# Optimization experiments

Hardware: AMD Instinct MI355X
Metric: run time of the kernel (lower is better)

## Reference

```python
import jax, jax.numpy as jnp
import numpy as np

F_NODES = 360        # nodes per graph == num_features (square connectome)
NUM_GRAPHS = 128
NUM_EDGES = 1_000_000
C = 128              # hidden_channels
NUM_LAYERS = 3
HIDDEN = 512
NUM_CLASSES = 2
EPS = 1e-5


def _bn(x, g, b):
    # BatchNorm1d in training mode: biased batch statistics over the batch dim.
    m = x.mean(axis=0)
    v = x.var(axis=0)
    return (x - m) * jax.lax.rsqrt(v + EPS) * g + b


def _gcn(x, W, b, src, dst):
    # GCNConv: x' = D^{-1/2} (A + I) D^{-1/2} (x W) + b
    N = x.shape[0]
    h = x @ W                                   # [N, C]
    loop = jnp.arange(N, dtype=src.dtype)
    src2 = jnp.concatenate([src, loop])
    dst2 = jnp.concatenate([dst, loop])
    deg = jax.ops.segment_sum(jnp.ones_like(dst2, dtype=h.dtype), dst2, num_segments=N)
    dinv = jnp.where(deg > 0, jax.lax.rsqrt(deg), 0.0)
    norm = dinv[src2] * dinv[dst2]              # [E+N]
    out = jax.ops.segment_sum(h[src2] * norm[:, None], dst2, num_segments=N)
    return out + b


def setup_inputs() -> dict:
    key = jax.random.key(0)
    ks = jax.random.split(key, 16)
    N = NUM_GRAPHS * F_NODES
    x = jax.random.normal(ks[0], (N, F_NODES), jnp.float32)
    # edges confined within each graph
    g = jax.random.randint(ks[1], (NUM_EDGES,), 0, NUM_GRAPHS)
    edge_src = g * F_NODES + jax.random.randint(ks[2], (NUM_EDGES,), 0, F_NODES)
    edge_dst = g * F_NODES + jax.random.randint(ks[3], (NUM_EDGES,), 0, F_NODES)
    batch = jnp.repeat(jnp.arange(NUM_GRAPHS), F_NODES)

    def lin(k, fi, fo):
        s = 1.0 / np.sqrt(fi)
        return jax.random.uniform(k, (fi, fo), jnp.float32, -s, s)

    input_dim = F_NODES * (F_NODES + 1) // 2    # 64980
    input_dim1 = input_dim + C * NUM_LAYERS     # 65364
    H2 = HIDDEN // 2
    params = dict(
        Wc1=lin(ks[4], F_NODES, C), bc1=jnp.zeros((C,), jnp.float32),
        Wc2=lin(ks[5], C, C), bc2=jnp.zeros((C,), jnp.float32),
        Wc3=lin(ks[6], C, C), bc3=jnp.zeros((C,), jnp.float32),
        bn_g=jnp.ones((input_dim,), jnp.float32), bn_b=jnp.zeros((input_dim,), jnp.float32),
        bnh_g=jnp.ones((C * NUM_LAYERS,), jnp.float32), bnh_b=jnp.zeros((C * NUM_LAYERS,), jnp.float32),
        W1=lin(ks[7], input_dim1, HIDDEN), b1=jnp.zeros((HIDDEN,), jnp.float32),
        g1=jnp.ones((HIDDEN,), jnp.float32), be1=jnp.zeros((HIDDEN,), jnp.float32),
        W2=lin(ks[8], HIDDEN, H2), b2=jnp.zeros((H2,), jnp.float32),
        g2=jnp.ones((H2,), jnp.float32), be2=jnp.zeros((H2,), jnp.float32),
        W3=lin(ks[9], H2, H2), b3=jnp.zeros((H2,), jnp.float32),
        g3=jnp.ones((H2,), jnp.float32), be3=jnp.zeros((H2,), jnp.float32),
        W4=lin(ks[10], H2, NUM_CLASSES), b4=jnp.zeros((NUM_CLASSES,), jnp.float32),
    )
    return {"x": x, "edge_src": edge_src, "edge_dst": edge_dst, "batch": batch, **params}


def reference(x, edge_src, edge_dst, batch,
              Wc1, bc1, Wc2, bc2, Wc3, bc3,
              bn_g, bn_b, bnh_g, bnh_b,
              W1, b1, g1, be1, W2, b2, g2, be2, W3, b3, g3, be3, W4, b4):
    N, F = x.shape
    B = N // F                                   # nodes per graph == F
    # stacked GCN convs with tanh
    xs = [x]
    for W, b in ((Wc1, bc1), (Wc2, bc2), (Wc3, bc3)):
        xs.append(jnp.tanh(_gcn(xs[-1], W, b, edge_src, edge_dst)))
    # per-graph upper-triangular gather of the raw connectome (vectorized)
    iu0, iu1 = np.triu_indices(F)
    x0 = xs[0].reshape(B, F, F)[:, iu0, iu1]     # [B, F(F+1)/2]
    x0 = _bn(x0, bn_g, bn_b)
    # per-layer segment-mean pooling over graphs
    cnt = jax.ops.segment_sum(jnp.ones((N,), x.dtype), batch, num_segments=B)
    h = jnp.concatenate(
        [jax.ops.segment_sum(xx, batch, num_segments=B) / cnt[:, None] for xx in xs[1:]],
        axis=1)                                  # [B, C*num_layers]
    h = _bn(h, bnh_g, bnh_b)
    z = jnp.concatenate([x0, h], axis=1)         # [B, input_dim1]
    # MLP head (dropout in eval mode => identity)
    z = jax.nn.relu(_bn(z @ W1 + b1, g1, be1))
    z = jax.nn.relu(_bn(z @ W2 + b2, g2, be2))
    z = jax.nn.relu(_bn(z @ W3 + b3, g3, be3))
    return jax.nn.log_softmax(z @ W4 + b4, axis=1)
```

## Files before the change

kernel.cpp:

```cpp
#include <hip/hip_runtime.h>
#include <hip/hip_bf16.h>
#include <math.h>

#define FN 360
#define NG 128
#define NN 46080
#define CH 128
#define NE 1000000
#define TRI 64980
#define D1 65364
#define ZLD 65376
#define H1 512
#define H2 256
#define EPS 1e-5f
#define NSPLIT 128

typedef unsigned short u16;
typedef __attribute__((ext_vector_type(8))) short bf16x8;
typedef __attribute__((ext_vector_type(4))) float f32x4;

__device__ __forceinline__ float bf2f(u16 v) {
  union { unsigned u; float f; } x; x.u = ((unsigned)v) << 16; return x.f;
}
__device__ __forceinline__ u16 f2bf(float f) {
  union { float f; unsigned u; } x; x.f = f;
  unsigned r = x.u + 0x7fffu + ((x.u >> 16) & 1u);
  return (u16)(r >> 16);
}
__device__ __forceinline__ bf16x8 bzero8() {
  bf16x8 z;
#pragma unroll
  for (int j = 0; j < 8; j++) z[j] = 0;
  return z;
}

static const size_t A32_OFF  = 0;
static const size_t DINV_OFF = 66355200;
static const size_t Z_OFF    = 66539520;
static const size_t PT_OFF   = 83275776;
static const size_t H1_OFF   = 95072256;
static const size_t H2_OFF   = 106868736;
static const size_t H3_OFF   = 118665216;
static const size_t HP_OFF   = 130461696;
static const size_t A1_OFF   = 130658304;
static const size_t A2_OFF   = 130789376;
static const size_t A3_OFF   = 130854912;
static const size_t Y1_OFF   = 130920448;
static const size_t PART_OFF = 0;

__global__ void k_deg(const int* __restrict__ dst, float* __restrict__ deg) {
  int e = blockIdx.x * 256 + threadIdx.x;
  if (e < NE) atomicAdd(&deg[dst[e]], 1.0f);
}

__global__ void k_dinv(float* __restrict__ deg) {
  int i = blockIdx.x * 256 + threadIdx.x;
  if (i < NN) deg[i] = rsqrtf(deg[i] + 1.0f);
}

__global__ void k_abuild(const int* __restrict__ src, const int* __restrict__ dst,
                         const float* __restrict__ dinv, float* __restrict__ A) {
  int e = blockIdx.x * 256 + threadIdx.x;
  if (e < NE) {
    int s = src[e], d = dst[e];
    int g = d / FN;
    int ls = s - g * FN, ld = d - g * FN;
    atomicAdd(&A[(size_t)g * FN * FN + (size_t)ld * FN + ls], dinv[s] * dinv[d]);
  } else if (e < NE + NN) {
    int i = e - NE;
    int g = i / FN, l = i - g * FN;
    float dv = dinv[i];
    atomicAdd(&A[(size_t)g * FN * FN + (size_t)l * FN + l], dv * dv);
  }
}

__global__ __launch_bounds__(256) void k_gemm_xw_f32(
    const float* __restrict__ X, const float* __restrict__ W,
    u16* __restrict__ PT, int K) {
  __shared__ __attribute__((aligned(16))) u16 WT[128][40];
  int wid = threadIdx.x >> 6, lane = threadIdx.x & 63;
  int quad = lane >> 4, l16 = lane & 15;
  int m0 = blockIdx.x * 64 + (wid & 1) * 32;
  int n0w = (wid >> 1) * 64;
  int kl = threadIdx.x >> 3, nseg = (threadIdx.x & 7) * 16;
  f32x4 acc[2][4];
#pragma unroll
  for (int i = 0; i < 2; i++)
#pragma unroll
    for (int j = 0; j < 4; j++) acc[i][j] = (f32x4){0,0,0,0};
  for (int k0 = 0; k0 < K; k0 += 32) {
    __syncthreads();
    int kg = k0 + kl;
    if (kg < K) {
      const float* wrow = W + (size_t)kg * CH + nseg;
      f32x4 w0 = *(const f32x4*)(wrow);
      f32x4 w1 = *(const f32x4*)(wrow + 4);
      f32x4 w2 = *(const f32x4*)(wrow + 8);
      f32x4 w3 = *(const f32x4*)(wrow + 12);
#pragma unroll
      for (int j = 0; j < 4; j++) {
        WT[nseg + j][kl]      = f2bf(w0[j]);
        WT[nseg + 4 + j][kl]  = f2bf(w1[j]);
        WT[nseg + 8 + j][kl]  = f2bf(w2[j]);
        WT[nseg + 12 + j][kl] = f2bf(w3[j]);
      }
    } else {
#pragma unroll
      for (int j = 0; j < 16; j++) WT[nseg + j][kl] = 0;
    }
    __syncthreads();
    int kk = k0 + quad * 8;
    bool kin = kk < K;
    bf16x8 af[2];
#pragma unroll
    for (int tm = 0; tm < 2; tm++) {
      int row = m0 + tm * 16 + l16;
      bf16x8 a = bzero8();
      if (kin) {
        f32x4 va = *(const f32x4*)(X + (size_t)row * K + kk);
        f32x4 vb = *(const f32x4*)(X + (size_t)row * K + kk + 4);
#pragma unroll
        for (int j = 0; j < 4; j++) { a[j] = (short)f2bf(va[j]); a[4 + j] = (short)f2bf(vb[j]); }
      }
      af[tm] = a;
    }
    bf16x8 bfr[4];
#pragma unroll
    for (int tn = 0; tn < 4; tn++)
      bfr[tn] = *(const bf16x8*)&WT[n0w + tn * 16 + l16][quad * 8];
#pragma unroll
    for (int tm = 0; tm < 2; tm++)
#pragma unroll
      for (int tn = 0; tn < 4; tn++)
        acc[tm][tn] = __builtin_amdgcn_mfma_f32_16x16x32_bf16(af[tm], bfr[tn], acc[tm][tn], 0, 0, 0);
  }
#pragma unroll
  for (int tm = 0; tm < 2; tm++)
#pragma unroll
    for (int tn = 0; tn < 4; tn++) {
      int col = n0w + tn * 16 + l16;
      int rowb = m0 + tm * 16 + quad * 4;
#pragma unroll
      for (int r = 0; r < 4; r++) {
        int row = rowb + r;
        int g = row / FN, lr = row - g * FN;
        PT[((size_t)g * CH + col) * FN + lr] = f2bf(acc[tm][tn][r]);
      }
    }
}

__global__ __launch_bounds__(256) void k_gemm_xw_bf16(
    const u16* __restrict__ X, const float* __restrict__ W,
    u16* __restrict__ PT) {
  __shared__ __attribute__((aligned(16))) u16 WT[128][40];
  int wid = threadIdx.x >> 6, lane = threadIdx.x & 63;
  int quad = lane >> 4, l16 = lane & 15;
  int m0 = blockIdx.x * 64 + (wid & 1) * 32;
  int n0w = (wid >> 1) * 64;
  int kl = threadIdx.x >> 3, nseg = (threadIdx.x & 7) * 16;
  f32x4 acc[2][4];
#pragma unroll
  for (int i = 0; i < 2; i++)
#pragma unroll
    for (int j = 0; j < 4; j++) acc[i][j] = (f32x4){0,0,0,0};
  for (int k0 = 0; k0 < CH; k0 += 32) {
    __syncthreads();
    int kg = k0 + kl;
    const float* wrow = W + (size_t)kg * CH + nseg;
    f32x4 w0 = *(const f32x4*)(wrow);
    f32x4 w1 = *(const f32x4*)(wrow + 4);
    f32x4 w2 = *(const f32x4*)(wrow + 8);
    f32x4 w3 = *(const f32x4*)(wrow + 12);
#pragma unroll
    for (int j = 0; j < 4; j++) {
      WT[nseg + j][kl]      = f2bf(w0[j]);
      WT[nseg + 4 + j][kl]  = f2bf(w1[j]);
      WT[nseg + 8 + j][kl]  = f2bf(w2[j]);
      WT[nseg + 12 + j][kl] = f2bf(w3[j]);
    }
    __syncthreads();
    int kk = k0 + quad * 8;
    bf16x8 af[2];
#pragma unroll
    for (int tm = 0; tm < 2; tm++) {
      int row = m0 + tm * 16 + l16;
      af[tm] = *(const bf16x8*)(X + (size_t)row * CH + kk);
    }
    bf16x8 bfr[4];
#pragma unroll
    for (int tn = 0; tn < 4; tn++)
      bfr[tn] = *(const bf16x8*)&WT[n0w + tn * 16 + l16][quad * 8];
#pragma unroll
    for (int tm = 0; tm < 2; tm++)
#pragma unroll
      for (int tn = 0; tn < 4; tn++)
        acc[tm][tn] = __builtin_amdgcn_mfma_f32_16x16x32_bf16(af[tm], bfr[tn], acc[tm][tn], 0, 0, 0);
  }
#pragma unroll
  for (int tm = 0; tm < 2; tm++)
#pragma unroll
    for (int tn = 0; tn < 4; tn++) {
      int col = n0w + tn * 16 + l16;
      int rowb = m0 + tm * 16 + quad * 4;
#pragma unroll
      for (int r = 0; r < 4; r++) {
        int row = rowb + r;
        int g = row / FN, lr = row - g * FN;
        PT[((size_t)g * CH + col) * FN + lr] = f2bf(acc[tm][tn][r]);
      }
    }
}

__global__ __launch_bounds__(256) void k_gemm_agg(
    const float* __restrict__ A32, const u16* __restrict__ PT,
    const float* __restrict__ bias, u16* __restrict__ Hout) {
  int id = blockIdx.x;
  int g = (id & 7) + 8 * (id / 48);
  int mb = (id % 48) >> 3;
  int wid = threadIdx.x >> 6, lane = threadIdx.x & 63;
  int quad = lane >> 4, l16 = lane & 15;
  int m0 = mb * 64 + (wid & 1) * 32;
  int n0 = (wid >> 1) * 64;
  const float* Ag = A32 + (size_t)g * FN * FN;
  const u16* PTg = PT + (size_t)g * CH * FN;
  f32x4 acc[2][4];
#pragma unroll
  for (int i = 0; i < 2; i++)
#pragma unroll
    for (int j = 0; j < 4; j++) acc[i][j] = (f32x4){0,0,0,0};
  for (int k0 = 0; k0 < FN; k0 += 32) {
    int kk = k0 + quad * 8;
    bool kin = kk < FN;
    bf16x8 af[2];
#pragma unroll
    for (int tm = 0; tm < 2; tm++) {
      int row = m0 + tm * 16 + l16;
      bf16x8 a = bzero8();
      if (kin && row < FN) {
        f32x4 va = *(const f32x4*)(Ag + (size_t)row * FN + kk);
        f32x4 vb = *(const f32x4*)(Ag + (size_t)row * FN + kk + 4);
#pragma unroll
        for (int j = 0; j < 4; j++) { a[j] = (short)f2bf(va[j]); a[4 + j] = (short)f2bf(vb[j]); }
      }
      af[tm] = a;
    }
    bf16x8 bfr[4];
#pragma unroll
    for (int tn = 0; tn < 4; tn++) {
      int col = n0 + tn * 16 + l16;
      bfr[tn] = kin ? *(const bf16x8*)(PTg + (size_t)col * FN + kk) : bzero8();
    }
#pragma unroll
    for (int tm = 0; tm < 2; tm++)
#pragma unroll
      for (int tn = 0; tn < 4; tn++)
        acc[tm][tn] = __builtin_amdgcn_mfma_f32_16x16x32_bf16(af[tm], bfr[tn], acc[tm][tn], 0, 0, 0);
  }
#pragma unroll
  for (int tm = 0; tm < 2; tm++)
#pragma unroll
    for (int tn = 0; tn < 4; tn++) {
      int col = n0 + tn * 16 + l16;
      float bc = bias[col];
      int rowb = m0 + tm * 16 + quad * 4;
#pragma unroll
      for (int r = 0; r < 4; r++) {
        int row = rowb + r;
        if (row < FN)
          Hout[(size_t)(g * FN + row) * CH + col] = f2bf(tanhf(acc[tm][tn][r] + bc));
      }
    }
}

__global__ __launch_bounds__(256) void k_gemm_big(
    const u16* __restrict__ Z, const float* __restrict__ W1f, float* __restrict__ part) {
  __shared__ __attribute__((aligned(16))) u16 WT[128][40];
  int id = blockIdx.x;
  int s = (id & 7) + 8 * (id >> 5);
  int n0b = ((id >> 3) & 3) * 128;
  int wid = threadIdx.x >> 6, lane = threadIdx.x & 63;
  int quad = lane >> 4, l16 = lane & 15;
  int m0 = wid * 32;
  int kl = threadIdx.x >> 3, nseg = (threadIdx.x & 7) * 16;
  int kbeg = s * 512;
  int kend = (ZLD < kbeg + 512) ? ZLD : (kbeg + 512);
  f32x4 acc[2][8];
#pragma unroll
  for (int i = 0; i < 2; i++)
#pragma unroll
    for (int j = 0; j < 8; j++) acc[i][j] = (f32x4){0,0,0,0};
  for (int k0 = kbeg; k0 < kend; k0 += 32) {
    __syncthreads();
    int kg = k0 + kl;
    if (kg < D1) {
      const float* wrow = W1f + (size_t)kg * H1 + n0b + nseg;
      f32x4 w0 = *(const f32x4*)(wrow);
      f32x4 w1 = *(const f32x4*)(wrow + 4);
      f32x4 w2 = *(const f32x4*)(wrow + 8);
      f32x4 w3 = *(const f32x4*)(wrow + 12);
#pragma unroll
      for (int j = 0; j < 4; j++) {
        WT[nseg + j][kl]      = f2bf(w0[j]);
        WT[nseg + 4 + j][kl]  = f2bf(w1[j]);
        WT[nseg + 8 + j][kl]  = f2bf(w2[j]);
        WT[nseg + 12 + j][kl] = f2bf(w3[j]);
      }
    } else {
#pragma unroll
      for (int j = 0; j < 16; j++) WT[nseg + j][kl] = 0;
    }
    __syncthreads();
    int kk = k0 + quad * 8;
    bf16x8 af[2];
#pragma unroll
    for (int tm = 0; tm < 2; tm++) {
      int row = m0 + tm * 16 + l16;
      af[tm] = *(const bf16x8*)(Z + (size_t)row * ZLD + kk);
    }
    bf16x8 bfr[8];
#pragma unroll
    for (int tn = 0; tn < 8; tn++)
      bfr[tn] = *(const bf16x8*)&WT[tn * 16 + l16][quad * 8];
#pragma unroll
    for (int tm = 0; tm < 2; tm++)
#pragma unroll
      for (int tn = 0; tn < 8; tn++)
        acc[tm][tn] = __builtin_amdgcn_mfma_f32_16x16x32_bf16(af[tm], bfr[tn], acc[tm][tn], 0, 0, 0);
  }
#pragma unroll
  for (int tm = 0; tm < 2; tm++)
#pragma unroll
    for (int tn = 0; tn < 8; tn++) {
      int col = n0b + tn * 16 + l16;
      int rowb = m0 + tm * 16 + quad * 4;
#pragma unroll
      for (int r = 0; r < 4; r++)
        part[((size_t)s * NG + rowb + r) * H1 + col] = acc[tm][tn][r];
    }
}

__global__ void k_red(const float* __restrict__ part, float* __restrict__ y1) {
  int idx = blockIdx.x * 256 + threadIdx.x;
  float s = 0.f;
#pragma unroll 8
  for (int i = 0; i < NSPLIT; i++) s += part[(size_t)i * 65536 + idx];
  y1[idx] = s;
}

__global__ __launch_bounds__(256) void k_bnrelu(
    const float* __restrict__ y, const float* __restrict__ gam,
    const float* __restrict__ bet, u16* __restrict__ a, int N) {
  __shared__ float sb[4][64], sb2[4][64];
  int c63 = threadIdx.x & 63;
  int grp = threadIdx.x >> 6;
  int c = blockIdx.x * 64 + c63;
  float s = 0.f, ss = 0.f;
#pragma unroll 8
  for (int m = grp * 32; m < grp * 32 + 32; m++) {
    float v = y[(size_t)m * N + c]; s += v; ss += v * v;
  }
  sb[grp][c63] = s; sb2[grp][c63] = ss;
  __syncthreads();
  float S = sb[0][c63] + sb[1][c63] + sb[2][c63] + sb[3][c63];
  float SS = sb2[0][c63] + sb2[1][c63] + sb2[2][c63] + sb2[3][c63];
  float mean = S * (1.0f / NG);
  float var = fmaxf(SS * (1.0f / NG) - mean * mean, 0.f);
  float rstd = rsqrtf(var + EPS);
  float ga = gam[c] * rstd;
  float bb = bet[c] - mean * ga;
#pragma unroll 8
  for (int m = grp * 32; m < grp * 32 + 32; m++) {
    float v = y[(size_t)m * N + c] * ga + bb;
    a[(size_t)m * N + c] = f2bf(fmaxf(v, 0.f));
  }
}

__global__ __launch_bounds__(256) void k_mlpbn(
    const u16* __restrict__ A, const float* __restrict__ W,
    const float* __restrict__ gam, const float* __restrict__ bet,
    u16* __restrict__ aout, int K, int N) {
  __shared__ __attribute__((aligned(16))) u16 WT[64][40];
  __shared__ float rs[4][4][4][16], rss[4][4][4][16];
  int wid = threadIdx.x >> 6, lane = threadIdx.x & 63;
  int quad = lane >> 4, l16 = lane & 15;
  int n0b = blockIdx.x * 64;
  int m0 = wid * 32;
  int kl = threadIdx.x >> 3;
  int nseg = (threadIdx.x & 7) * 8;
  f32x4 acc[2][4];
#pragma unroll
  for (int i = 0; i < 2; i++)
#pragma unroll
    for (int j = 0; j < 4; j++) acc[i][j] = (f32x4){0,0,0,0};
  for (int k0 = 0; k0 < K; k0 += 32) {
    __syncthreads();
    const float* wrow = W + (size_t)(k0 + kl) * N + n0b + nseg;
    f32x4 w0 = *(const f32x4*)(wrow);
    f32x4 w1 = *(const f32x4*)(wrow + 4);
#pragma unroll
    for (int j = 0; j < 4; j++) {
      WT[nseg + j][kl]     = f2bf(w0[j]);
      WT[nseg + 4 + j][kl] = f2bf(w1[j]);
    }
    __syncthreads();
    int kk = k0 + quad * 8;
    bf16x8 af[2];
#pragma unroll
    for (int tm = 0; tm < 2; tm++) {
      int row = m0 + tm * 16 + l16;
      af[tm] = *(const bf16x8*)(A + (size_t)row * K + kk);
    }
    bf16x8 bfr[4];
#pragma unroll
    for (int tn = 0; tn < 4; tn++)
      bfr[tn] = *(const bf16x8*)&WT[tn * 16 + l16][quad * 8];
#pragma unroll
    for (int tm = 0; tm < 2; tm++)
#pragma unroll
      for (int tn = 0; tn < 4; tn++)
        acc[tm][tn] = __builtin_amdgcn_mfma_f32_16x16x32_bf16(af[tm], bfr[tn], acc[tm][tn], 0, 0, 0);
  }
  __syncthreads();
#pragma unroll
  for (int tn = 0; tn < 4; tn++) {
    float s = 0.f, ss = 0.f;
#pragma unroll
    for (int tm = 0; tm < 2; tm++)
#pragma unroll
      for (int r = 0; r < 4; r++) { float v = acc[tm][tn][r]; s += v; ss += v * v; }
    rs[wid][quad][tn][l16] = s;
    rss[wid][quad][tn][l16] = ss;
  }
  __syncthreads();
#pragma unroll
  for (int tn = 0; tn < 4; tn++) {
    float S = 0.f, SS = 0.f;
#pragma unroll
    for (int w = 0; w < 4; w++)
#pragma unroll
      for (int q = 0; q < 4; q++) { S += rs[w][q][tn][l16]; SS += rss[w][q][tn][l16]; }
    float mean = S * (1.0f / NG);
    float var = fmaxf(SS * (1.0f / NG) - mean * mean, 0.f);
    float rstd = rsqrtf(var + EPS);
    int col = n0b + tn * 16 + l16;
    float ga = gam[col] * rstd;
    float bb = bet[col] - mean * ga;
#pragma unroll
    for (int tm = 0; tm < 2; tm++) {
      int rowb = m0 + tm * 16 + quad * 4;
#pragma unroll
      for (int r = 0; r < 4; r++) {
        float v = acc[tm][tn][r] * ga + bb;
        aout[(size_t)(rowb + r) * N + col] = f2bf(fmaxf(v, 0.f));
      }
    }
  }
}

__global__ void k_pool3(const u16* __restrict__ h1, const u16* __restrict__ h2,
                        const u16* __restrict__ h3, float* __restrict__ hp) {
  int g = blockIdx.x, layer = blockIdx.y, c = threadIdx.x;
  const u16* h = (layer == 0) ? h1 : (layer == 1) ? h2 : h3;
  float s = 0.f;
#pragma unroll 8
  for (int r = 0; r < FN; r++) s += bf2f(h[(size_t)(g * FN + r) * CH + c]);
  hp[g * 384 + layer * CH + c] = s * (1.0f / FN);
}

__global__ __launch_bounds__(256) void k_x0bn(
    const float* __restrict__ x, const float* __restrict__ gam,
    const float* __restrict__ bet, const float* __restrict__ hp,
    const float* __restrict__ hgam, const float* __restrict__ hbet,
    u16* __restrict__ z) {
  int i = blockIdx.x;
  if (i < FN) {
    int off = i * FN - (i * (i - 1)) / 2;
    for (int j = i + (int)threadIdx.x; j < FN; j += 256) {
      float s = 0.f, ss = 0.f;
#pragma unroll 8
      for (int b = 0; b < NG; b++) {
        float v = x[(size_t)(b * FN + i) * FN + j];
        s += v; ss += v * v;
      }
      float mean = s * (1.0f / NG);
      float var = fmaxf(ss * (1.0f / NG) - mean * mean, 0.f);
      float rstd = rsqrtf(var + EPS);
      int f = off + (j - i);
      float ga = gam[f] * rstd;
      float bb = bet[f] - mean * ga;
#pragma unroll 8
      for (int b = 0; b < NG; b++) {
        float v = x[(size_t)(b * FN + i) * FN + j];
        z[(size_t)b * ZLD + f] = f2bf(v * ga + bb);
      }
    }
  } else {
    for (int c = threadIdx.x; c < 384; c += 256) {
      float s = 0.f, ss = 0.f;
#pragma unroll 8
      for (int m = 0; m < NG; m++) { float v = hp[m * 384 + c]; s += v; ss += v * v; }
      float mean = s * (1.0f / NG);
      float var = fmaxf(ss * (1.0f / NG) - mean * mean, 0.f);
      float rstd = rsqrtf(var + EPS);
      float ga = hgam[c] * rstd;
      float bb = hbet[c] - mean * ga;
#pragma unroll 8
      for (int m = 0; m < NG; m++)
        z[(size_t)m * ZLD + TRI + c] = f2bf(hp[m * 384 + c] * ga + bb);
    }
    if (threadIdx.x < NG) {
      for (int t = 0; t < ZLD - D1; t++)
        z[(size_t)threadIdx.x * ZLD + D1 + t] = 0;
    }
  }
}

__global__ void k_head(const u16* __restrict__ a3, const float* __restrict__ W4,
                       const float* __restrict__ b4, float* __restrict__ out) {
  __shared__ float w4s[H2 * 2];
  int m = threadIdx.x;
  for (int i = m; i < H2 * 2; i += 128) w4s[i] = W4[i];
  __syncthreads();
  float a0 = b4[0], a1 = b4[1];
  for (int k0 = 0; k0 < H2; k0 += 8) {
    bf16x8 v = *(const bf16x8*)(a3 + (size_t)m * H2 + k0);
#pragma unroll
    for (int j = 0; j < 8; j++) {
      float f = bf2f((u16)v[j]);
      a0 += f * w4s[(k0 + j) * 2];
      a1 += f * w4s[(k0 + j) * 2 + 1];
    }
  }
  float mx = fmaxf(a0, a1);
  float lse = mx + logf(expf(a0 - mx) + expf(a1 - mx));
  out[m * 2]     = a0 - lse;
  out[m * 2 + 1] = a1 - lse;
}

extern "C" void kernel_launch(void* const* d_in, const int* in_sizes, int n_in,
                              void* d_out, int out_size, void* d_ws, size_t ws_size,
                              hipStream_t stream) {
  const float* x    = (const float*)d_in[0];
  const int* esrc   = (const int*)d_in[1];
  const int* edst   = (const int*)d_in[2];
  const float* Wc1 = (const float*)d_in[4];  const float* bc1 = (const float*)d_in[5];
  const float* Wc2 = (const float*)d_in[6];  const float* bc2 = (const float*)d_in[7];
  const float* Wc3 = (const float*)d_in[8];  const float* bc3 = (const float*)d_in[9];
  const float* bn_g = (const float*)d_in[10]; const float* bn_b = (const float*)d_in[11];
  const float* bnh_g = (const float*)d_in[12]; const float* bnh_b = (const float*)d_in[13];
  const float* W1 = (const float*)d_in[14];
  const float* g1 = (const float*)d_in[16]; const float* be1 = (const float*)d_in[17];
  const float* W2 = (const float*)d_in[18];
  const float* g2 = (const float*)d_in[20]; const float* be2 = (const float*)d_in[21];
  const float* W3 = (const float*)d_in[22];
  const float* g3 = (const float*)d_in[24]; const float* be3 = (const float*)d_in[25];
  const float* W4 = (const float*)d_in[26]; const float* b4 = (const float*)d_in[27];

  char* ws = (char*)d_ws;
  float* A32  = (float*)(ws + A32_OFF);
  float* dinv = (float*)(ws + DINV_OFF);
  u16*   z    = (u16*)(ws + Z_OFF);
  u16*   PT   = (u16*)(ws + PT_OFF);
  u16*   h1   = (u16*)(ws + H1_OFF);
  u16*   h2   = (u16*)(ws + H2_OFF);
  u16*   h3   = (u16*)(ws + H3_OFF);
  float* hp   = (float*)(ws + HP_OFF);
  u16*   a1   = (u16*)(ws + A1_OFF);
  u16*   a2   = (u16*)(ws + A2_OFF);
  u16*   a3   = (u16*)(ws + A3_OFF);
  float* y1   = (float*)(ws + Y1_OFF);
  float* part = (float*)(ws + PART_OFF);

  (void)hipMemsetAsync(A32, 0, (size_t)NG * FN * FN * 4 + (size_t)NN * 4, stream);

  dim3 b256(256);
  k_deg<<<dim3((NE + 255) / 256), b256, 0, stream>>>(edst, dinv);
  k_dinv<<<dim3((NN + 255) / 256), b256, 0, stream>>>(dinv);
  k_abuild<<<dim3((NE + NN + 255) / 256), b256, 0, stream>>>(esrc, edst, dinv, A32);

  k_gemm_xw_f32<<<dim3(NN / 64), b256, 0, stream>>>(x, Wc1, PT, FN);
  k_gemm_agg<<<dim3(NG * 6), b256, 0, stream>>>(A32, PT, bc1, h1);
  k_gemm_xw_bf16<<<dim3(NN / 64), b256, 0, stream>>>(h1, Wc2, PT);
  k_gemm_agg<<<dim3(NG * 6), b256, 0, stream>>>(A32, PT, bc2, h2);
  k_gemm_xw_bf16<<<dim3(NN / 64), b256, 0, stream>>>(h2, Wc3, PT);
  k_gemm_agg<<<dim3(NG * 6), b256, 0, stream>>>(A32, PT, bc3, h3);

  k_pool3<<<dim3(NG, 3), dim3(128), 0, stream>>>(h1, h2, h3, hp);
  k_x0bn<<<dim3(FN + 1), b256, 0, stream>>>(x, bn_g, bn_b, hp, bnh_g, bnh_b, z);

  k_gemm_big<<<dim3(512), b256, 0, stream>>>(z, W1, part);
  k_red<<<dim3(65536 / 256), b256, 0, stream>>>(part, y1);
  k_bnrelu<<<dim3(H1 / 64), b256, 0, stream>>>(y1, g1, be1, a1, H1);
  k_mlpbn<<<dim3(H2 / 64), b256, 0, stream>>>(a1, W2, g2, be2, a2, H1, H2);
  k_mlpbn<<<dim3(H2 / 64), b256, 0, stream>>>(a2, W3, g3, be3, a3, H2, H2);
  k_head<<<dim3(1), dim3(128), 0, stream>>>(a3, W4, b4, (float*)d_out);
}
```

Measured before the change: 665.7 us.

## Fuse pooling into aggregation, cache bf16 adjacency, fold dinv into abuild

The first aggregation kernel now also writes a bf16 copy of the normalized adjacency, so layers 2 and 3 read half the bytes instead of re-reading and re-converting the fp32 matrix. Per-graph mean pooling moves into the aggregation epilogue through shared-memory partial sums and atomics, which removes the separate pool kernel and the third hidden-state write. The dinv kernel is dropped and rsqrt is computed inline in abuild. The workspace is re-laid out so buffers are reused, and the memset grows to zero the pooled accumulator, at the cost of atomic order nondeterminism in the pooled sums.

```diff
diff --git a/kernel.cpp b/kernel.cpp
--- a/kernel.cpp
+++ b/kernel.cpp
@@ -35,41 +35,36 @@
 }
 
 static const size_t A32_OFF  = 0;
-static const size_t DINV_OFF = 66355200;
-static const size_t Z_OFF    = 66539520;
-static const size_t PT_OFF   = 83275776;
-static const size_t H1_OFF   = 95072256;
-static const size_t H2_OFF   = 106868736;
-static const size_t H3_OFF   = 118665216;
-static const size_t HP_OFF   = 130461696;
-static const size_t A1_OFF   = 130658304;
-static const size_t A2_OFF   = 130789376;
-static const size_t A3_OFF   = 130854912;
-static const size_t Y1_OFF   = 130920448;
-static const size_t PART_OFF = 0;
+static const size_t Z_OFF    = 0;
+static const size_t PART_OFF = 16736256;
+static const size_t Y1_OFF   = 50290688;
+static const size_t A1_OFF   = 50552832;
+static const size_t A2_OFF   = 50683904;
+static const size_t A3_OFF   = 50749440;
+static const size_t DEG_OFF  = 66355200;
+static const size_t HP_OFF   = 66539520;
+static const size_t AB_OFF   = 66736128;
+static const size_t PT_OFF   = 99913728;
+static const size_t H_OFF    = 111710208;
 
 __global__ void k_deg(const int* __restrict__ dst, float* __restrict__ deg) {
   int e = blockIdx.x * 256 + threadIdx.x;
   if (e < NE) atomicAdd(&deg[dst[e]], 1.0f);
 }
 
-__global__ void k_dinv(float* __restrict__ deg) {
-  int i = blockIdx.x * 256 + threadIdx.x;
-  if (i < NN) deg[i] = rsqrtf(deg[i] + 1.0f);
-}
-
 __global__ void k_abuild(const int* __restrict__ src, const int* __restrict__ dst,
-                         const float* __restrict__ dinv, float* __restrict__ A) {
+                         const float* __restrict__ deg, float* __restrict__ A) {
   int e = blockIdx.x * 256 + threadIdx.x;
   if (e < NE) {
     int s = src[e], d = dst[e];
     int g = d / FN;
     int ls = s - g * FN, ld = d - g * FN;
-    atomicAdd(&A[(size_t)g * FN * FN + (size_t)ld * FN + ls], dinv[s] * dinv[d]);
+    float w = rsqrtf(deg[s] + 1.0f) * rsqrtf(deg[d] + 1.0f);
+    atomicAdd(&A[(size_t)g * FN * FN + (size_t)ld * FN + ls], w);
   } else if (e < NE + NN) {
     int i = e - NE;
     int g = i / FN, l = i - g * FN;
-    float dv = dinv[i];
+    float dv = rsqrtf(deg[i] + 1.0f);
     atomicAdd(&A[(size_t)g * FN * FN + (size_t)l * FN + l], dv * dv);
   }
 }
@@ -211,9 +206,11 @@
     }
 }
 
-__global__ __launch_bounds__(256) void k_gemm_agg(
+__global__ __launch_bounds__(256) void k_agg1(
     const float* __restrict__ A32, const u16* __restrict__ PT,
-    const float* __restrict__ bias, u16* __restrict__ Hout) {
+    const float* __restrict__ bias, u16* __restrict__ Hout,
+    u16* __restrict__ Ab, float* __restrict__ hp) {
+  __shared__ float ps[8][128];
   int id = blockIdx.x;
   int g = (id & 7) + 8 * (id / 48);
   int mb = (id % 48) >> 3;
@@ -222,7 +219,9 @@
   int m0 = mb * 64 + (wid & 1) * 32;
   int n0 = (wid >> 1) * 64;
   const float* Ag = A32 + (size_t)g * FN * FN;
+  u16* Abg = Ab + (size_t)g * FN * FN;
   const u16* PTg = PT + (size_t)g * CH * FN;
+  bool wr_ab = ((wid >> 1) == 0);
   f32x4 acc[2][4];
 #pragma unroll
   for (int i = 0; i < 2; i++)
@@ -241,6 +240,7 @@
         f32x4 vb = *(const f32x4*)(Ag + (size_t)row * FN + kk + 4);
 #pragma unroll
         for (int j = 0; j < 4; j++) { a[j] = (short)f2bf(va[j]); a[4 + j] = (short)f2bf(vb[j]); }
+        if (wr_ab) *(bf16x8*)(Abg + (size_t)row * FN + kk) = a;
       }
       af[tm] = a;
     }
@@ -256,6 +256,7 @@
       for (int tn = 0; tn < 4; tn++)
         acc[tm][tn] = __builtin_amdgcn_mfma_f32_16x16x32_bf16(af[tm], bfr[tn], acc[tm][tn], 0, 0, 0);
   }
+  float lsum[4] = {0.f, 0.f, 0.f, 0.f};
 #pragma unroll
   for (int tm = 0; tm < 2; tm++)
 #pragma unroll
@@ -266,10 +267,93 @@
 #pragma unroll
       for (int r = 0; r < 4; r++) {
         int row = rowb + r;
-        if (row < FN)
-          Hout[(size_t)(g * FN + row) * CH + col] = f2bf(tanhf(acc[tm][tn][r] + bc));
-      }
-    }
+        if (row < FN) {
+          float t = tanhf(acc[tm][tn][r] + bc);
+          Hout[(size_t)(g * FN + row) * CH + col] = f2bf(t);
+          lsum[tn] += t;
+        }
+      }
+    }
+  int cid = (wid & 1) * 4 + quad;
+#pragma unroll
+  for (int tn = 0; tn < 4; tn++) ps[cid][n0 + tn * 16 + l16] = lsum[tn];
+  __syncthreads();
+  if (threadIdx.x < 128) {
+    float s = 0.f;
+#pragma unroll
+    for (int c = 0; c < 8; c++) s += ps[c][threadIdx.x];
+    atomicAdd(&hp[g * 384 + threadIdx.x], s);
+  }
+}
+
+__global__ __launch_bounds__(256) void k_agg23(
+    const u16* __restrict__ Ab, const u16* __restrict__ PT,
+    const float* __restrict__ bias, u16* __restrict__ Hout,
+    float* __restrict__ hp, int loff) {
+  __shared__ float ps[8][128];
+  int id = blockIdx.x;
+  int g = (id & 7) + 8 * (id / 48);
+  int mb = (id % 48) >> 3;
+  int wid = threadIdx.x >> 6, lane = threadIdx.x & 63;
+  int quad = lane >> 4, l16 = lane & 15;
+  int m0 = mb * 64 + (wid & 1) * 32;
+  int n0 = (wid >> 1) * 64;
+  const u16* Abg = Ab + (size_t)g * FN * FN;
+  const u16* PTg = PT + (size_t)g * CH * FN;
+  f32x4 acc[2][4];
+#pragma unroll
+  for (int i = 0; i < 2; i++)
+#pragma unroll
+    for (int j = 0; j < 4; j++) acc[i][j] = (f32x4){0,0,0,0};
+  for (int k0 = 0; k0 < FN; k0 += 32) {
+    int kk = k0 + quad * 8;
+    bool kin = kk < FN;
+    bf16x8 af[2];
+#pragma unroll
+    for (int tm = 0; tm < 2; tm++) {
+      int row = m0 + tm * 16 + l16;
+      af[tm] = (kin && row < FN) ? *(const bf16x8*)(Abg + (size_t)row * FN + kk) : bzero8();
+    }
+    bf16x8 bfr[4];
+#pragma unroll
+    for (int tn = 0; tn < 4; tn++) {
+      int col = n0 + tn * 16 + l16;
+      bfr[tn] = kin ? *(const bf16x8*)(PTg + (size_t)col * FN + kk) : bzero8();
+    }
+#pragma unroll
+    for (int tm = 0; tm < 2; tm++)
+#pragma unroll
+      for (int tn = 0; tn < 4; tn++)
+        acc[tm][tn] = __builtin_amdgcn_mfma_f32_16x16x32_bf16(af[tm], bfr[tn], acc[tm][tn], 0, 0, 0);
+  }
+  float lsum[4] = {0.f, 0.f, 0.f, 0.f};
+#pragma unroll
+  for (int tm = 0; tm < 2; tm++)
+#pragma unroll
+    for (int tn = 0; tn < 4; tn++) {
+      int col = n0 + tn * 16 + l16;
+      float bc = bias[col];
+      int rowb = m0 + tm * 16 + quad * 4;
+#pragma unroll
+      for (int r = 0; r < 4; r++) {
+        int row = rowb + r;
+        if (row < FN) {
+          float t = tanhf(acc[tm][tn][r] + bc);
+          if (Hout) Hout[(size_t)(g * FN + row) * CH + col] = f2bf(t);
+          lsum[tn] += t;
+        }
+      }
+    }
+  int cid = (wid & 1) * 4 + quad;
+#pragma unroll
+  for (int tn = 0; tn < 4; tn++) ps[cid][n0 + tn * 16 + l16] = lsum[tn];
+  __syncthreads();
+  if (threadIdx.x < 128) {
+    float s = 0.f;
+#pragma unroll
+    for (int c = 0; c < 8; c++) s += ps[c][threadIdx.x];
+    atomicAdd(&hp[g * 384 + loff + threadIdx.x], s);
+  }
 }
 
 __global__ __launch_bounds__(256) void k_gemm_big(
@@ -455,16 +539,6 @@
       }
     }
   }
-}
-
-__global__ void k_pool3(const u16* __restrict__ h1, const u16* __restrict__ h2,
-                        const u16* __restrict__ h3, float* __restrict__ hp) {
-  int g = blockIdx.x, layer = blockIdx.y, c = threadIdx.x;
-  const u16* h = (layer == 0) ? h1 : (layer == 1) ? h2 : h3;
-  float s = 0.f;
-#pragma unroll 8
-  for (int r = 0; r < FN; r++) s += bf2f(h[(size_t)(g * FN + r) * CH + c]);
-  hp[g * 384 + layer * CH + c] = s * (1.0f / FN);
 }
 
 __global__ __launch_bounds__(256) void k_x0bn(
@@ -498,7 +572,10 @@
     for (int c = threadIdx.x; c < 384; c += 256) {
       float s = 0.f, ss = 0.f;
 #pragma unroll 8
-      for (int m = 0; m < NG; m++) { float v = hp[m * 384 + c]; s += v; ss += v * v; }
+      for (int m = 0; m < NG; m++) {
+        float v = hp[m * 384 + c] * (1.0f / FN);
+        s += v; ss += v * v;
+      }
       float mean = s * (1.0f / NG);
       float var = fmaxf(ss * (1.0f / NG) - mean * mean, 0.f);
       float rstd = rsqrtf(var + EPS);
@@ -506,7 +583,7 @@
       float bb = hbet[c] - mean * ga;
 #pragma unroll 8
       for (int m = 0; m < NG; m++)
-        z[(size_t)m * ZLD + TRI + c] = f2bf(hp[m * 384 + c] * ga + bb);
+        z[(size_t)m * ZLD + TRI + c] = f2bf(hp[m * 384 + c] * (1.0f / FN) * ga + bb);
     }
     if (threadIdx.x < NG) {
       for (int t = 0; t < ZLD - D1; t++)
@@ -558,34 +635,31 @@
 
   char* ws = (char*)d_ws;
   float* A32  = (float*)(ws + A32_OFF);
-  float* dinv = (float*)(ws + DINV_OFF);
+  float* deg  = (float*)(ws + DEG_OFF);
+  float* hp   = (float*)(ws + HP_OFF);
+  u16*   Ab   = (u16*)(ws + AB_OFF);
+  u16*   PT   = (u16*)(ws + PT_OFF);
+  u16*   h    = (u16*)(ws + H_OFF);
   u16*   z    = (u16*)(ws + Z_OFF);
-  u16*   PT   = (u16*)(ws + PT_OFF);
-  u16*   h1   = (u16*)(ws + H1_OFF);
-  u16*   h2   = (u16*)(ws + H2_OFF);
-  u16*   h3   = (u16*)(ws + H3_OFF);
-  float* hp   = (float*)(ws + HP_OFF);
+  float* part = (float*)(ws + PART_OFF);
+  float* y1   = (float*)(ws + Y1_OFF);
   u16*   a1   = (u16*)(ws + A1_OFF);
   u16*   a2   = (u16*)(ws + A2_OFF);
   u16*   a3   = (u16*)(ws + A3_OFF);
-  float* y1   = (float*)(ws + Y1_OFF);
-  float* part = (float*)(ws + PART_OFF);
-
-  (void)hipMemsetAsync(A32, 0, (size_t)NG * FN * FN * 4 + (size_t)NN * 4, stream);
+
+  (void)hipMemsetAsync(A32, 0, (size_t)NG * FN * FN * 4 + (size_t)NN * 4 + (size_t)NG * 384 * 4, stream);
 
   dim3 b256(256);
-  k_deg<<<dim3((NE + 255) / 256), b256, 0, stream>>>(edst, dinv);
-  k_dinv<<<dim3((NN + 255) / 256), b256, 0, stream>>>(dinv);
-  k_abuild<<<dim3((NE + NN + 255) / 256), b256, 0, stream>>>(esrc, edst, dinv, A32);
+  k_deg<<<dim3((NE + 255) / 256), b256, 0, stream>>>(edst, deg);
+  k_abuild<<<dim3((NE + NN + 255) / 256), b256, 0, stream>>>(esrc, edst, deg, A32);
 
   k_gemm_xw_f32<<<dim3(NN / 64), b256, 0, stream>>>(x, Wc1, PT, FN);
-  k_gemm_agg<<<dim3(NG * 6), b256, 0, stream>>>(A32, PT, bc1, h1);
-  k_gemm_xw_bf16<<<dim3(NN / 64), b256, 0, stream>>>(h1, Wc2, PT);
-  k_gemm_agg<<<dim3(NG * 6), b256, 0, stream>>>(A32, PT, bc2, h2);
-  k_gemm_xw_bf16<<<dim3(NN / 64), b256, 0, stream>>>(h2, Wc3, PT);
-  k_gemm_agg<<<dim3(NG * 6), b256, 0, stream>>>(A32, PT, bc3, h3);
-
-  k_pool3<<<dim3(NG, 3), dim3(128), 0, stream>>>(h1, h2, h3, hp);
+  k_agg1<<<dim3(NG * 6), b256, 0, stream>>>(A32, PT, bc1, h, Ab, hp);
+  k_gemm_xw_bf16<<<dim3(NN / 64), b256, 0, stream>>>(h, Wc2, PT);
+  k_agg23<<<dim3(NG * 6), b256, 0, stream>>>(Ab, PT, bc2, h, hp, CH);
+  k_gemm_xw_bf16<<<dim3(NN / 64), b256, 0, stream>>>(h, Wc3, PT);
+  k_agg23<<<dim3(NG * 6), b256, 0, stream>>>(Ab, PT, bc3, (u16*)nullptr, hp, 2 * CH);
+
   k_x0bn<<<dim3(FN + 1), b256, 0, stream>>>(x, bn_g, bn_b, hp, bnh_g, bnh_b, z);
 
   k_gemm_big<<<dim3(512), b256, 0, stream>>>(z, W1, part);
```

New measurement: 648.1 us. 1.03x faster.
